# Optimization experiments

Measured on AMD Instinct MI355X. Metric: run time of the kernel, lower is better.

## Reference

```python
import jax, jax.numpy as jnp
import numpy as np


def setup_inputs() -> dict:
    key = jax.random.key(0)
    k1, k2 = jax.random.split(key)
    b, t, d = 4, 2048, 1024
    x = jax.random.normal(k1, (b, t, d), dtype=jnp.float32)
    # torch Linear weight has shape [out_features, in_features] = [3*d, d]
    W_qkv = jax.random.normal(k2, (3 * d, d), dtype=jnp.float32) * (2.0 / (d + 3 * d)) ** 0.5
    return {"x": x, "W_qkv": W_qkv}


def reference(x, W_qkv):
    b, t, d = x.shape
    scale = d ** -0.5
    qkv = jnp.einsum('btd,ed->bte', x, W_qkv)          # [b, t, 3d]
    # rearrange 'b t (d k) -> k b t d' with k=3: last axis splits as (d, 3)
    qkv = qkv.reshape(b, t, d, 3)
    q, k, v = qkv[..., 0], qkv[..., 1], qkv[..., 2]     # each [b, t, d]
    scores = jnp.einsum('bid,bjd->bij', q, k) * scale   # [b, t, t]
    attn = jax.nn.softmax(scores, axis=-1)
    return jnp.einsum('bij,bjd->bid', attn, v)          # [b, t, d]
```

## Files before the change

### kernel.cpp

```cpp
#include <hip/hip_runtime.h>
#include <math.h>

#define NBATCH 4
#define TDIM 2048
#define DDIM 1024

typedef __attribute__((ext_vector_type(8))) short short8;
typedef __attribute__((ext_vector_type(4))) float floatx4;
typedef __attribute__((ext_vector_type(8))) unsigned short ushort8;
typedef __attribute__((ext_vector_type(4))) unsigned short ushort4v;

__device__ __forceinline__ unsigned short f2bf(float f) {
  unsigned int u = __float_as_uint(f);
  u += 0x7fffu + ((u >> 16) & 1u);
  return (unsigned short)(u >> 16);
}
__device__ __forceinline__ float bf2f(unsigned short h) {
  return __uint_as_float(((unsigned int)h) << 16);
}

__device__ __forceinline__ void gload_lds16(const ushort* g, ushort* l) {
  __builtin_amdgcn_global_load_lds(
      (const __attribute__((address_space(1))) void*)g,
      (__attribute__((address_space(3))) void*)l, 16, 0, 0);
}

__device__ __forceinline__ void mfma_gemm_core(
    const ushort* __restrict__ Abase, const ushort* __restrict__ Bbase,
    int lda, int ldb, int K, ushort* As, ushort* Bs, floatx4 acc[4][4]) {
  const int tid = threadIdx.x;
  const int wave = tid >> 6;
  const int lane = tid & 63;
  const int l15 = lane & 15;
  const int quad = lane >> 4;
  const int wm = wave >> 1, wn = wave & 1;

  const int srow = wave * 32 + (lane >> 3);
  const int schunk = (lane & 7) ^ ((lane >> 3) & 7);
  const ushort* ag = Abase + (size_t)srow * lda + schunk * 8;
  const ushort* bg = Bbase + (size_t)srow * ldb + schunk * 8;
  ushort* al = As + wave * 32 * 64;
  ushort* bl = Bs + wave * 32 * 64;

  const int slot = quad ^ (l15 & 7);
  const int abase = (wm * 64 + l15) * 64 + slot * 8;
  const int bbase = (wn * 64 + l15) * 64 + slot * 8;

  for (int kt = 0; kt < K; kt += 64) {
#pragma unroll
    for (int i = 0; i < 4; ++i) {
      gload_lds16(ag + kt + (size_t)(8 * i) * lda, al + 8 * i * 64);
      gload_lds16(bg + kt + (size_t)(8 * i) * ldb, bl + 8 * i * 64);
    }
    __syncthreads();
#pragma unroll
    for (int g = 0; g < 2; ++g) {
      const int ab = abase ^ (g * 32);
      const int bb = bbase ^ (g * 32);
      short8 af[4], bfr[4];
#pragma unroll
      for (int t = 0; t < 4; ++t) {
        af[t] = *(const short8*)&As[ab + t * 1024];
        bfr[t] = *(const short8*)&Bs[bb + t * 1024];
      }
#pragma unroll
      for (int i = 0; i < 4; ++i)
#pragma unroll
        for (int j = 0; j < 4; ++j)
          acc[i][j] =
              __builtin_amdgcn_mfma_f32_16x16x32_bf16(af[i], bfr[j], acc[i][j], 0, 0, 0);
    }
    __syncthreads();
  }
}

__global__ __launch_bounds__(256) void convert_xw(
    const float* __restrict__ x, const float* __restrict__ W,
    ushort* __restrict__ xb, ushort* __restrict__ wb) {
  const int bid = blockIdx.x;
  if (bid < 8192) {
    const size_t i = (size_t)bid * 256 + threadIdx.x;
    float4 v = reinterpret_cast<const float4*>(x)[i];
    ushort4v h = {f2bf(v.x), f2bf(v.y), f2bf(v.z), f2bf(v.w)};
    reinterpret_cast<ushort4v*>(xb)[i] = h;
  } else {
    const int e = bid - 8192;
    const int c = e % 3, ii = e / 3;
    const float scale = (c == 0) ? 0.03125f : 1.0f;
    const float4 v = reinterpret_cast<const float4*>(W + (size_t)e * DDIM)[threadIdx.x];
    ushort4v h = {f2bf(v.x * scale), f2bf(v.y * scale), f2bf(v.z * scale),
                  f2bf(v.w * scale)};
    reinterpret_cast<ushort4v*>(wb + (size_t)(c * DDIM + ii) * DDIM)[threadIdx.x] = h;
  }
}

__global__ __launch_bounds__(256, 3) void qkv_gemm(
    const ushort* __restrict__ xb, const ushort* __restrict__ wb,
    ushort* __restrict__ qb, ushort* __restrict__ kb, ushort* __restrict__ vt) {
  __shared__ __align__(16) ushort As[128 * 64];
  __shared__ __align__(16) ushort Bs[128 * 64];
  const int m0 = blockIdx.y * 128;
  const int n0 = blockIdx.x * 128;
  floatx4 acc[4][4];
  const floatx4 z4 = {0.f, 0.f, 0.f, 0.f};
#pragma unroll
  for (int i = 0; i < 4; ++i)
#pragma unroll
    for (int j = 0; j < 4; ++j) acc[i][j] = z4;

  mfma_gemm_core(xb + (size_t)m0 * DDIM, wb + (size_t)n0 * DDIM, DDIM, DDIM,
                 DDIM, As, Bs, acc);

  const int tid = threadIdx.x;
  const int wave = tid >> 6, lane = tid & 63;
  const int l15 = lane & 15, quad = lane >> 4;
  const int wm = wave >> 1, wn = wave & 1;

  if (n0 < 2 * DDIM) {
    ushort* dst = (n0 < DDIM) ? qb : kb;
    const int cb = (n0 < DDIM) ? n0 : n0 - DDIM;
#pragma unroll
    for (int i = 0; i < 4; ++i) {
      const int rbase = m0 + wm * 64 + i * 16 + quad * 4;
#pragma unroll
      for (int j = 0; j < 4; ++j) {
        const int col = cb + wn * 64 + j * 16 + l15;
#pragma unroll
        for (int r = 0; r < 4; ++r)
          dst[(size_t)(rbase + r) * DDIM + col] = f2bf(acc[i][j][r]);
      }
    }
  } else {
#pragma unroll
    for (int i = 0; i < 4; ++i) {
      const int row = m0 + wm * 64 + i * 16 + quad * 4;
      const int b = row >> 11, t = row & (TDIM - 1);
#pragma unroll
      for (int j = 0; j < 4; ++j) {
        const int d = (n0 - 2 * DDIM) + wn * 64 + j * 16 + l15;
        ushort4v pk = {f2bf(acc[i][j][0]), f2bf(acc[i][j][1]),
                       f2bf(acc[i][j][2]), f2bf(acc[i][j][3])};
        *reinterpret_cast<ushort4v*>(&vt[(size_t)((b << 10) + d) * TDIM + t]) = pk;
      }
    }
  }
}

__global__ __launch_bounds__(256, 3) void score_gemm(
    const ushort* __restrict__ qb, const ushort* __restrict__ kb,
    ushort* __restrict__ Sb) {
  __shared__ __align__(16) ushort As[128 * 64];
  __shared__ __align__(16) ushort Bs[128 * 64];
  const int z = blockIdx.z;
  const int m0 = blockIdx.y * 128;
  const int n0 = blockIdx.x * 128;
  floatx4 acc[4][4];
  const floatx4 z4 = {0.f, 0.f, 0.f, 0.f};
#pragma unroll
  for (int i = 0; i < 4; ++i)
#pragma unroll
    for (int j = 0; j < 4; ++j) acc[i][j] = z4;

  mfma_gemm_core(qb + ((size_t)z * TDIM + m0) * DDIM,
                 kb + ((size_t)z * TDIM + n0) * DDIM, DDIM, DDIM, DDIM, As, Bs,
                 acc);

  const int tid = threadIdx.x;
  const int wave = tid >> 6, lane = tid & 63;
  const int l15 = lane & 15, quad = lane >> 4;
  const int wm = wave >> 1, wn = wave & 1;
  ushort* S = Sb + (size_t)z * TDIM * TDIM;
#pragma unroll
  for (int i = 0; i < 4; ++i) {
    const int rbase = m0 + wm * 64 + i * 16 + quad * 4;
#pragma unroll
    for (int j = 0; j < 4; ++j) {
      const int col = n0 + wn * 64 + j * 16 + l15;
#pragma unroll
      for (int r = 0; r < 4; ++r)
        S[(size_t)(rbase + r) * TDIM + col] = f2bf(acc[i][j][r]);
    }
  }
}

__global__ __launch_bounds__(256) void softmax_rows(ushort* __restrict__ Sb) {
  __shared__ float redm[4], reds[4];
  const int tid = threadIdx.x;
  ushort* p = Sb + (size_t)blockIdx.x * TDIM;
  ushort8 hv = *reinterpret_cast<const ushort8*>(&p[tid * 8]);
  float x[8];
#pragma unroll
  for (int e = 0; e < 8; ++e) x[e] = bf2f(hv[e]);

  float m = x[0];
#pragma unroll
  for (int e = 1; e < 8; ++e) m = fmaxf(m, x[e]);
#pragma unroll
  for (int off = 32; off > 0; off >>= 1) m = fmaxf(m, __shfl_down(m, off, 64));
  const int wave = tid >> 6, lane = tid & 63;
  if (lane == 0) redm[wave] = m;
  __syncthreads();
  m = fmaxf(fmaxf(redm[0], redm[1]), fmaxf(redm[2], redm[3]));

  float s = 0.f;
#pragma unroll
  for (int e = 0; e < 8; ++e) {
    x[e] = __expf(x[e] - m);
    s += x[e];
  }
#pragma unroll
  for (int off = 32; off > 0; off >>= 1) s += __shfl_down(s, off, 64);
  if (lane == 0) reds[wave] = s;
  __syncthreads();
  s = reds[0] + reds[1] + reds[2] + reds[3];
  const float inv = 1.0f / s;
#pragma unroll
  for (int e = 0; e < 8; ++e) hv[e] = f2bf(x[e] * inv);
  *reinterpret_cast<ushort8*>(&p[tid * 8]) = hv;
}

__global__ __launch_bounds__(256, 3) void pv_gemm(
    const ushort* __restrict__ Pb, const ushort* __restrict__ vt,
    float* __restrict__ out) {
  __shared__ __align__(16) ushort As[128 * 64];
  __shared__ __align__(16) ushort Bs[128 * 64];
  const int z = blockIdx.z;
  const int m0 = blockIdx.y * 128;
  const int n0 = blockIdx.x * 128;
  floatx4 acc[4][4];
  const floatx4 z4 = {0.f, 0.f, 0.f, 0.f};
#pragma unroll
  for (int i = 0; i < 4; ++i)
#pragma unroll
    for (int j = 0; j < 4; ++j) acc[i][j] = z4;

  mfma_gemm_core(Pb + (size_t)z * TDIM * TDIM + (size_t)m0 * TDIM,
                 vt + (size_t)z * DDIM * TDIM + (size_t)n0 * TDIM, TDIM, TDIM,
                 TDIM, As, Bs, acc);

  const int tid = threadIdx.x;
  const int wave = tid >> 6, lane = tid & 63;
  const int l15 = lane & 15, quad = lane >> 4;
  const int wm = wave >> 1, wn = wave & 1;
  float* O = out + (size_t)z * TDIM * DDIM;
#pragma unroll
  for (int i = 0; i < 4; ++i) {
    const int rbase = m0 + wm * 64 + i * 16 + quad * 4;
#pragma unroll
    for (int j = 0; j < 4; ++j) {
      const int col = n0 + wn * 64 + j * 16 + l15;
#pragma unroll
      for (int r = 0; r < 4; ++r)
        O[(size_t)(rbase + r) * DDIM + col] = acc[i][j][r];
    }
  }
}

extern "C" void kernel_launch(void* const* d_in, const int* in_sizes, int n_in,
                              void* d_out, int out_size, void* d_ws, size_t ws_size,
                              hipStream_t stream) {
  const float* x = (const float*)d_in[0];
  const float* W = (const float*)d_in[1];
  float* out = (float*)d_out;

  ushort* ws = (ushort*)d_ws;
  const size_t n_x = (size_t)NBATCH * TDIM * DDIM;
  const size_t n_w = (size_t)3 * DDIM * DDIM;
  ushort* xb = ws;
  ushort* wb = xb + n_x;
  ushort* qb = wb + n_w;
  ushort* kb = qb + n_x;
  ushort* vt = kb + n_x;
  ushort* Sb = vt + n_x;

  convert_xw<<<dim3(8192 + 3 * DDIM), 256, 0, stream>>>(x, W, xb, wb);
  qkv_gemm<<<dim3(3 * DDIM / 128, NBATCH * TDIM / 128), 256, 0, stream>>>(
      xb, wb, qb, kb, vt);
  score_gemm<<<dim3(TDIM / 128, TDIM / 128, NBATCH), 256, 0, stream>>>(qb, kb, Sb);
  softmax_rows<<<dim3(NBATCH * TDIM), 256, 0, stream>>>(Sb);
  pv_gemm<<<dim3(DDIM / 128, TDIM / 128, NBATCH), 256, 0, stream>>>(Sb, vt, out);
}
```

Before: 237.5 us.

## Fuse all attention stages into one persistent cooperative kernel with grid syncs

Merges the convert, QKV GEMM, score GEMM, softmax and PV GEMM kernels into a single cooperative kernel of 512 persistent blocks. Each phase loops over its work units and is separated from the next by grid.sync(). This removes the launch overhead and tail gaps between the five kernels. The cost is lower occupancy (launch bounds of 2 blocks per CU, 512 blocks total), grid-barrier overhead, and a fixed block count that makes the earlier large-grid phases such as convert and softmax loop many times. If the cooperative launch fails, it falls back to separate kernels.

```diff
diff --git a/kernel.cpp b/kernel.cpp
--- a/kernel.cpp
+++ b/kernel.cpp
@@ -1,9 +1,13 @@
 #include <hip/hip_runtime.h>
+#include <hip/hip_cooperative_groups.h>
 #include <math.h>
+
+namespace cg = cooperative_groups;
 
 #define NBATCH 4
 #define TDIM 2048
 #define DDIM 1024
+#define NPERSIST 512
 
 typedef __attribute__((ext_vector_type(8))) short short8;
 typedef __attribute__((ext_vector_type(4))) float floatx4;
@@ -74,33 +78,36 @@
   }
 }
 
-__global__ __launch_bounds__(256) void convert_xw(
-    const float* __restrict__ x, const float* __restrict__ W,
-    ushort* __restrict__ xb, ushort* __restrict__ wb) {
-  const int bid = blockIdx.x;
-  if (bid < 8192) {
-    const size_t i = (size_t)bid * 256 + threadIdx.x;
+
+__device__ __forceinline__ void phase_convert(int u, int tid,
+                                              const float* __restrict__ x,
+                                              const float* __restrict__ W,
+                                              ushort* __restrict__ xb,
+                                              ushort* __restrict__ wb) {
+  if (u < 8192) {
+    const size_t i = (size_t)u * 256 + tid;
     float4 v = reinterpret_cast<const float4*>(x)[i];
     ushort4v h = {f2bf(v.x), f2bf(v.y), f2bf(v.z), f2bf(v.w)};
     reinterpret_cast<ushort4v*>(xb)[i] = h;
   } else {
-    const int e = bid - 8192;
+    const int e = u - 8192;
     const int c = e % 3, ii = e / 3;
     const float scale = (c == 0) ? 0.03125f : 1.0f;
-    const float4 v = reinterpret_cast<const float4*>(W + (size_t)e * DDIM)[threadIdx.x];
+    const float4 v = reinterpret_cast<const float4*>(W + (size_t)e * DDIM)[tid];
     ushort4v h = {f2bf(v.x * scale), f2bf(v.y * scale), f2bf(v.z * scale),
                   f2bf(v.w * scale)};
-    reinterpret_cast<ushort4v*>(wb + (size_t)(c * DDIM + ii) * DDIM)[threadIdx.x] = h;
-  }
-}
-
-__global__ __launch_bounds__(256, 3) void qkv_gemm(
-    const ushort* __restrict__ xb, const ushort* __restrict__ wb,
-    ushort* __restrict__ qb, ushort* __restrict__ kb, ushort* __restrict__ vt) {
-  __shared__ __align__(16) ushort As[128 * 64];
-  __shared__ __align__(16) ushort Bs[128 * 64];
-  const int m0 = blockIdx.y * 128;
-  const int n0 = blockIdx.x * 128;
+    reinterpret_cast<ushort4v*>(wb + (size_t)(c * DDIM + ii) * DDIM)[tid] = h;
+  }
+}
+
+__device__ __forceinline__ void phase_qkv(int u, const ushort* __restrict__ xb,
+                                          const ushort* __restrict__ wb,
+                                          ushort* __restrict__ qb,
+                                          ushort* __restrict__ kb,
+                                          ushort* __restrict__ vt, ushort* As,
+                                          ushort* Bs) {
+  const int m0 = (u / 24) * 128;
+  const int n0 = (u % 24) * 128;
   floatx4 acc[4][4];
   const floatx4 z4 = {0.f, 0.f, 0.f, 0.f};
 #pragma unroll
@@ -146,14 +153,13 @@
   }
 }
 
-__global__ __launch_bounds__(256, 3) void score_gemm(
-    const ushort* __restrict__ qb, const ushort* __restrict__ kb,
-    ushort* __restrict__ Sb) {
-  __shared__ __align__(16) ushort As[128 * 64];
-  __shared__ __align__(16) ushort Bs[128 * 64];
-  const int z = blockIdx.z;
-  const int m0 = blockIdx.y * 128;
-  const int n0 = blockIdx.x * 128;
+__device__ __forceinline__ void phase_score(int u, const ushort* __restrict__ qb,
+                                            const ushort* __restrict__ kb,
+                                            ushort* __restrict__ Sb, ushort* As,
+                                            ushort* Bs) {
+  const int z = u >> 8;
+  const int m0 = ((u & 255) >> 4) * 128;
+  const int n0 = (u & 15) * 128;
   floatx4 acc[4][4];
   const floatx4 z4 = {0.f, 0.f, 0.f, 0.f};
 #pragma unroll
@@ -183,10 +189,10 @@
   }
 }
 
-__global__ __launch_bounds__(256) void softmax_rows(ushort* __restrict__ Sb) {
-  __shared__ float redm[4], reds[4];
-  const int tid = threadIdx.x;
-  ushort* p = Sb + (size_t)blockIdx.x * TDIM;
+__device__ __forceinline__ void phase_softmax(int row, int tid,
+                                              ushort* __restrict__ Sb,
+                                              float* red) {
+  ushort* p = Sb + (size_t)row * TDIM;
   ushort8 hv = *reinterpret_cast<const ushort8*>(&p[tid * 8]);
   float x[8];
 #pragma unroll
@@ -198,9 +204,9 @@
 #pragma unroll
   for (int off = 32; off > 0; off >>= 1) m = fmaxf(m, __shfl_down(m, off, 64));
   const int wave = tid >> 6, lane = tid & 63;
-  if (lane == 0) redm[wave] = m;
+  if (lane == 0) red[wave] = m;
   __syncthreads();
-  m = fmaxf(fmaxf(redm[0], redm[1]), fmaxf(redm[2], redm[3]));
+  m = fmaxf(fmaxf(red[0], red[1]), fmaxf(red[2], red[3]));
 
   float s = 0.f;
 #pragma unroll
@@ -210,23 +216,22 @@
   }
 #pragma unroll
   for (int off = 32; off > 0; off >>= 1) s += __shfl_down(s, off, 64);
-  if (lane == 0) reds[wave] = s;
+  if (lane == 0) red[4 + wave] = s;
   __syncthreads();
-  s = reds[0] + reds[1] + reds[2] + reds[3];
+  s = red[4] + red[5] + red[6] + red[7];
   const float inv = 1.0f / s;
 #pragma unroll
   for (int e = 0; e < 8; ++e) hv[e] = f2bf(x[e] * inv);
   *reinterpret_cast<ushort8*>(&p[tid * 8]) = hv;
 }
 
-__global__ __launch_bounds__(256, 3) void pv_gemm(
-    const ushort* __restrict__ Pb, const ushort* __restrict__ vt,
-    float* __restrict__ out) {
-  __shared__ __align__(16) ushort As[128 * 64];
-  __shared__ __align__(16) ushort Bs[128 * 64];
-  const int z = blockIdx.z;
-  const int m0 = blockIdx.y * 128;
-  const int n0 = blockIdx.x * 128;
+__device__ __forceinline__ void phase_pv(int u, const ushort* __restrict__ Pb,
+                                         const ushort* __restrict__ vt,
+                                         float* __restrict__ out, ushort* As,
+                                         ushort* Bs) {
+  const int z = u >> 7;
+  const int m0 = ((u & 127) >> 3) * 128;
+  const int n0 = (u & 7) * 128;
   floatx4 acc[4][4];
   const floatx4 z4 = {0.f, 0.f, 0.f, 0.f};
 #pragma unroll
@@ -254,6 +259,64 @@
         O[(size_t)(rbase + r) * DDIM + col] = acc[i][j][r];
     }
   }
+}
+
+__global__ __launch_bounds__(256, 2) void fused_attn(
+    const float* __restrict__ x, const float* __restrict__ W,
+    float* __restrict__ out, ushort* xb, ushort* wb, ushort* qb, ushort* kb,
+    ushort* vt, ushort* Sb) {
+  __shared__ __align__(16) ushort As[128 * 64];
+  __shared__ __align__(16) ushort Bs[128 * 64];
+  cg::grid_group grid = cg::this_grid();
+  const int bid = blockIdx.x;
+  const int tid = threadIdx.x;
+
+  for (int u = bid; u < 8192 + 3072; u += NPERSIST)
+    phase_convert(u, tid, x, W, xb, wb);
+  grid.sync();
+
+  for (int u = bid; u < 1536; u += NPERSIST)
+    phase_qkv(u, xb, wb, qb, kb, vt, As, Bs);
+  grid.sync();
+
+  for (int u = bid; u < 1024; u += NPERSIST)
+    phase_score(u, qb, kb, Sb, As, Bs);
+  grid.sync();
+
+  float* red = reinterpret_cast<float*>(As);
+  for (int row = bid; row < NBATCH * TDIM; row += NPERSIST)
+    phase_softmax(row, tid, Sb, red);
+  grid.sync();
+
+  phase_pv(bid, Sb, vt, out, As, Bs);
+}
+
+__global__ __launch_bounds__(256) void k_convert(const float* __restrict__ x,
+                                                 const float* __restrict__ W,
+                                                 ushort* xb, ushort* wb) {
+  phase_convert(blockIdx.x, threadIdx.x, x, W, xb, wb);
+}
+__global__ __launch_bounds__(256, 3) void k_qkv(const ushort* xb, const ushort* wb,
+                                                ushort* qb, ushort* kb, ushort* vt) {
+  __shared__ __align__(16) ushort As[128 * 64];
+  __shared__ __align__(16) ushort Bs[128 * 64];
+  phase_qkv(blockIdx.x, xb, wb, qb, kb, vt, As, Bs);
+}
+__global__ __launch_bounds__(256, 3) void k_score(const ushort* qb, const ushort* kb,
+                                                  ushort* Sb) {
+  __shared__ __align__(16) ushort As[128 * 64];
+  __shared__ __align__(16) ushort Bs[128 * 64];
+  phase_score(blockIdx.x, qb, kb, Sb, As, Bs);
+}
+__global__ __launch_bounds__(256) void k_softmax(ushort* Sb) {
+  __shared__ float red[8];
+  phase_softmax(blockIdx.x, threadIdx.x, Sb, red);
+}
+__global__ __launch_bounds__(256, 3) void k_pv(const ushort* Pb, const ushort* vt,
+                                               float* out) {
+  __shared__ __align__(16) ushort As[128 * 64];
+  __shared__ __align__(16) ushort Bs[128 * 64];
+  phase_pv(blockIdx.x, Pb, vt, out, As, Bs);
 }
 
 extern "C" void kernel_launch(void* const* d_in, const int* in_sizes, int n_in,
@@ -273,10 +336,17 @@
   ushort* vt = kb + n_x;
   ushort* Sb = vt + n_x;
 
-  convert_xw<<<dim3(8192 + 3 * DDIM), 256, 0, stream>>>(x, W, xb, wb);
-  qkv_gemm<<<dim3(3 * DDIM / 128, NBATCH * TDIM / 128), 256, 0, stream>>>(
-      xb, wb, qb, kb, vt);
-  score_gemm<<<dim3(TDIM / 128, TDIM / 128, NBATCH), 256, 0, stream>>>(qb, kb, Sb);
-  softmax_rows<<<dim3(NBATCH * TDIM), 256, 0, stream>>>(Sb);
-  pv_gemm<<<dim3(DDIM / 128, TDIM / 128, NBATCH), 256, 0, stream>>>(Sb, vt, out);
-}
+  void* args[] = {(void*)&x, (void*)&W, (void*)&out, (void*)&xb, (void*)&wb,
+                  (void*)&qb, (void*)&kb, (void*)&vt, (void*)&Sb};
+  hipError_t err = hipLaunchCooperativeKernel((const void*)fused_attn,
+                                              dim3(NPERSIST), dim3(256), args,
+                                              0, stream);
+  if (err != hipSuccess) {
+    (void)hipGetLastError();
+    k_convert<<<dim3(8192 + 3 * DDIM), 256, 0, stream>>>(x, W, xb, wb);
+    k_qkv<<<dim3(1536), 256, 0, stream>>>(xb, wb, qb, kb, vt);
+    k_score<<<dim3(1024), 256, 0, stream>>>(qb, kb, Sb);
+    k_softmax<<<dim3(NBATCH * TDIM), 256, 0, stream>>>(Sb);
+    k_pv<<<dim3(512), 256, 0, stream>>>(Sb, vt, out);
+  }
+}
```

Measured after the change: 525.5 us. +121.2%, slower.
